# Kernel optimization log

Hardware: AMD Instinct MI355X
Metric: run time of the kernel (lower is better)

## Reference

```python
import jax, jax.numpy as jnp
import numpy as np

D_MODEL = 1024
NUM_HEADS = 16
B, S = 2, 2048


def setup_inputs() -> dict:
    key = jax.random.key(0)
    ks = jax.random.split(key, 11)
    scale = 1.0 / np.sqrt(D_MODEL)
    inp = {
        'q': jax.random.normal(ks[0], (B, S, D_MODEL), jnp.float32),
        'k': jax.random.normal(ks[1], (B, S, D_MODEL), jnp.float32),
        'v': jax.random.normal(ks[2], (B, S, D_MODEL), jnp.float32),
        'w_q': jax.random.normal(ks[3], (D_MODEL, D_MODEL), jnp.float32) * scale,
        'b_q': jax.random.normal(ks[4], (D_MODEL,), jnp.float32) * 0.01,
        'w_k': jax.random.normal(ks[5], (D_MODEL, D_MODEL), jnp.float32) * scale,
        'b_k': jax.random.normal(ks[6], (D_MODEL,), jnp.float32) * 0.01,
        'w_v': jax.random.normal(ks[7], (D_MODEL, D_MODEL), jnp.float32) * scale,
        'b_v': jax.random.normal(ks[8], (D_MODEL,), jnp.float32) * 0.01,
        'w_o': jax.random.normal(ks[9], (D_MODEL, D_MODEL), jnp.float32) * scale,
        'b_o': jax.random.normal(ks[10], (D_MODEL,), jnp.float32) * 0.01,
    }
    return inp


def reference(q, k, v, w_q, b_q, w_k, b_k, w_v, b_v, w_o, b_o):
    Bq, Sq, D = q.shape
    H = NUM_HEADS
    dh = D // H
    # projections (weights stored as [in, out])
    query = q @ w_q + b_q
    key = k @ w_k + b_k
    value = v @ w_v + b_v
    # [B, S, D] -> [B, H, S, dh]
    query = query.reshape(Bq, Sq, H, dh).transpose(0, 2, 1, 3)
    key = key.reshape(Bq, -1, H, dh).transpose(0, 2, 1, 3)
    value = value.reshape(Bq, -1, H, dh).transpose(0, 2, 1, 3)
    # NOTE: original module does NOT scale by 1/sqrt(dh)
    scores = jnp.einsum('bhqd,bhkd->bhqk', query, key)  # [B,H,S,S]
    causal_mask = jnp.triu(jnp.ones((Sq, Sq), dtype=bool), k=1)  # True above diag
    scores = jnp.where(causal_mask[None, None], -jnp.inf, scores)
    attn = jax.nn.softmax(scores, axis=-1)
    data = jnp.einsum('bhqk,bhkd->bhqd', attn, value)  # [B,H,S,dh]
    # FAITHFUL to original bug: transpose(0,1) then view(B, S, -1)
    data = data.transpose(1, 0, 2, 3).reshape(Bq, Sq, -1)  # [H,B,S,dh] -> [B,S,D]
    return data @ w_o + b_o
```

## Files before the change

kernel.cpp:

```cpp
#include <hip/hip_runtime.h>

typedef __fp16 f16;
typedef __fp16 f16x8 __attribute__((ext_vector_type(8)));
typedef __fp16 f16x4 __attribute__((ext_vector_type(4)));
typedef __fp16 f16x2 __attribute__((ext_vector_type(2)));
typedef float f32x4 __attribute__((ext_vector_type(4)));
typedef float f32x16 __attribute__((ext_vector_type(16)));

#define D_MODEL 1024
#define SEQ 2048
#define NH 16
#define MTOT 4096

typedef const __attribute__((address_space(1))) unsigned int* gp1_t;
typedef __attribute__((address_space(3))) unsigned int* lp3_t;

__device__ __forceinline__ void gload_lds16(const void* g, void* l) {
  __builtin_amdgcn_global_load_lds((gp1_t)g, (lp3_t)l, 16, 0, 0);
}

__device__ __forceinline__ int permrow(int r) {
  int bp = r >> 11, u = (r >> 7) & 15, t = r & 127;
  int g16 = (bp << 4) | u;
  return ((((g16 & 1) << 4) | (g16 >> 1)) << 7) + t;
}

__device__ __forceinline__ unsigned int pkrtz(float a, float b) {
  union { f16x2 h; unsigned int u; } z;
  z.h = __builtin_amdgcn_cvt_pkrtz(a, b);
  return z.u;
}

__global__ __launch_bounds__(256) void cvt_all(const float* __restrict__ q,
                                               const float* __restrict__ k,
                                               const float* __restrict__ v,
                                               const float* __restrict__ wq,
                                               const float* __restrict__ wk,
                                               const float* __restrict__ wv,
                                               const float* __restrict__ wo,
                                               f16* __restrict__ qkv16,
                                               f16* __restrict__ wT) {
  __shared__ float tl[64][65];
  int bid = blockIdx.x, tid = threadIdx.x;
  if (bid < 6144) {
    int i = bid * 256 + tid;
    const int NT = (MTOT * D_MODEL) / 8;
    const float* src;
    int t;
    if (i < NT) { src = q; t = i; }
    else if (i < 2 * NT) { src = k; t = i - NT; }
    else { src = v; t = i - 2 * NT; }
    const float4* s4 = (const float4*)src;
    float4 a = s4[2 * t], b = s4[2 * t + 1];
    f16x8 h;
    h[0] = (f16)a.x; h[1] = (f16)a.y; h[2] = (f16)a.z; h[3] = (f16)a.w;
    h[4] = (f16)b.x; h[5] = (f16)b.y; h[6] = (f16)b.z; h[7] = (f16)b.w;
    *(f16x8*)(qkv16 + (size_t)i * 8) = h;
  } else {
    int bb = bid - 6144;
    int mat = bb >> 8, tile = bb & 255;
    int tk = (tile >> 4) << 6, tn = (tile & 15) << 6;
    const float* W = mat == 0 ? wq : mat == 1 ? wk : mat == 2 ? wv : wo;
    int rr = tid >> 4, c4 = (tid & 15) << 2;
#pragma unroll
    for (int it = 0; it < 4; ++it) {
      const float* p = W + (size_t)(tk + it * 16 + rr) * D_MODEL + tn + c4;
      float4 val = *(const float4*)p;
      tl[it * 16 + rr][c4 + 0] = val.x;
      tl[it * 16 + rr][c4 + 1] = val.y;
      tl[it * 16 + rr][c4 + 2] = val.z;
      tl[it * 16 + rr][c4 + 3] = val.w;
    }
    __syncthreads();
    int n = tid & 63, kseg = (tid >> 6) << 4;
    f16x8 lo, hi;
#pragma unroll
    for (int j = 0; j < 8; ++j) lo[j] = (f16)tl[kseg + j][n];
#pragma unroll
    for (int j = 0; j < 8; ++j) hi[j] = (f16)tl[kseg + 8 + j][n];
    f16* d = wT + (size_t)mat * (D_MODEL * D_MODEL) + (size_t)(tn + n) * D_MODEL + tk + kseg;
    *(f16x8*)d = lo;
    *(f16x8*)(d + 8) = hi;
  }
}

__global__ __launch_bounds__(256, 2) void gemm_qkv(const f16* __restrict__ q16,
                                                   const f16* __restrict__ k16,
                                                   const f16* __restrict__ v16,
                                                   const f16* __restrict__ wT,
                                                   const float* __restrict__ bq,
                                                   const float* __restrict__ bk,
                                                   const float* __restrict__ bv,
                                                   f16* __restrict__ Q16,
                                                   f16* __restrict__ K16,
                                                   f16* __restrict__ VT16) {
  const int K = D_MODEL, N = D_MODEL;
  const size_t WEL = (size_t)D_MODEL * D_MODEL;
  int z = blockIdx.z;
  const f16* A = z == 0 ? q16 : z == 1 ? k16 : v16;
  const f16* BT = wT + (size_t)z * WEL;
  const float* bias = z == 0 ? bq : z == 1 ? bk : bv;

  __shared__ f16 As[128 * 64];
  __shared__ f16 Bs[128 * 64];
  int tid = threadIdx.x;
  int w = tid >> 6, lane = tid & 63;
  int g = lane >> 4, c = lane & 15;
  int wr = w >> 1, wc = w & 1;
  int m0 = blockIdx.x * 128, n0 = blockIdx.y * 128;
  f32x4 acc[4][4] = {};

  for (int kt = 0; kt < K; kt += 64) {
#pragma unroll
    for (int i = 0; i < 4; ++i) {
      int seg = w * 4 + i;
      int p = seg * 1024 + lane * 16;
      int row = p >> 7;
      int colb = (p & 127) ^ ((row & 7) << 4);
      int ae = kt + (colb >> 1);
      gload_lds16(A + (size_t)(m0 + row) * K + ae, &As[seg * 512]);
      gload_lds16(BT + (size_t)(n0 + row) * K + ae, &Bs[seg * 512]);
    }
    __syncthreads();
    f16x8 af[4][2], bf[4][2];
#pragma unroll
    for (int m = 0; m < 4; ++m) {
#pragma unroll
      for (int kk = 0; kk < 2; ++kk) {
        int row = wr * 64 + m * 16 + c;
        int tb = (row * 128 + kk * 64 + g * 16) ^ ((row & 7) << 4);
        af[m][kk] = *(const f16x8*)((const char*)As + tb);
      }
    }
#pragma unroll
    for (int n = 0; n < 4; ++n) {
#pragma unroll
      for (int kk = 0; kk < 2; ++kk) {
        int row = wc * 64 + n * 16 + c;
        int tb = (row * 128 + kk * 64 + g * 16) ^ ((row & 7) << 4);
        bf[n][kk] = *(const f16x8*)((const char*)Bs + tb);
      }
    }
    __builtin_amdgcn_s_setprio(1);
#pragma unroll
    for (int m = 0; m < 4; ++m)
#pragma unroll
      for (int n = 0; n < 4; ++n)
#pragma unroll
        for (int kk = 0; kk < 2; ++kk)
          acc[m][n] = __builtin_amdgcn_mfma_f32_16x16x32_f16(af[m][kk], bf[n][kk], acc[m][n], 0, 0, 0);
    __builtin_amdgcn_s_setprio(0);
    __syncthreads();
  }

  int rb = m0 + wr * 64;
  int cb = n0 + wc * 64;
  if (z < 2) {
    f16* O = z == 0 ? Q16 : K16;
#pragma unroll
    for (int m = 0; m < 4; ++m) {
      int row0 = rb + m * 16 + 4 * g;
#pragma unroll
      for (int n = 0; n < 4; ++n) {
        int col = cb + n * 16 + c;
        float bv2 = bias[col];
#pragma unroll
        for (int r = 0; r < 4; ++r) O[(size_t)(row0 + r) * N + col] = (f16)(acc[m][n][r] + bv2);
      }
    }
  } else {
    f16* O = VT16;
#pragma unroll
    for (int m = 0; m < 4; ++m) {
      int s0f = rb + m * 16 + 4 * g;
      int bb = s0f >> 11, s = s0f & (SEQ - 1);
#pragma unroll
      for (int n = 0; n < 4; ++n) {
        int col = cb + n * 16 + c;
        float bv2 = bias[col];
        f16x4 hv;
#pragma unroll
        for (int r = 0; r < 4; ++r) hv[r] = (f16)(acc[m][n][r] + bv2);
        *(f16x4*)(O + ((size_t)(bb * NH + (col >> 6)) * 64 + (col & 63)) * SEQ + s) = hv;
      }
    }
  }
}

__global__ __launch_bounds__(256, 2) void gemm_out(const f16* __restrict__ A,
                                                   const f16* __restrict__ BT,
                                                   const float* __restrict__ bias,
                                                   float* __restrict__ O) {
  const int K = D_MODEL, N = D_MODEL;
  __shared__ f16 As[64 * 64];
  __shared__ f16 Bs[128 * 64];
  int tid = threadIdx.x;
  int w = tid >> 6, lane = tid & 63;
  int g = lane >> 4, c = lane & 15;
  int wr = w >> 1, wc = w & 1;
  int m0 = blockIdx.x * 64, n0 = blockIdx.y * 128;
  f32x4 acc[2][4] = {};

  for (int kt = 0; kt < K; kt += 64) {
#pragma unroll
    for (int i = 0; i < 2; ++i) {
      int seg = w * 2 + i;
      int p = seg * 1024 + lane * 16;
      int row = p >> 7;
      int colb = (p & 127) ^ ((row & 7) << 4);
      int ae = kt + (colb >> 1);
      gload_lds16(A + (size_t)permrow(m0 + row) * K + ae, &As[seg * 512]);
    }
#pragma unroll
    for (int i = 0; i < 4; ++i) {
      int seg = w * 4 + i;
      int p = seg * 1024 + lane * 16;
      int row = p >> 7;
      int colb = (p & 127) ^ ((row & 7) << 4);
      int ae = kt + (colb >> 1);
      gload_lds16(BT + (size_t)(n0 + row) * K + ae, &Bs[seg * 512]);
    }
    __syncthreads();
    f16x8 af[2][2], bf[4][2];
#pragma unroll
    for (int m = 0; m < 2; ++m) {
#pragma unroll
      for (int kk = 0; kk < 2; ++kk) {
        int row = wr * 32 + m * 16 + c;
        int tb = (row * 128 + kk * 64 + g * 16) ^ ((row & 7) << 4);
        af[m][kk] = *(const f16x8*)((const char*)As + tb);
      }
    }
#pragma unroll
    for (int n = 0; n < 4; ++n) {
#pragma unroll
      for (int kk = 0; kk < 2; ++kk) {
        int row = wc * 64 + n * 16 + c;
        int tb = (row * 128 + kk * 64 + g * 16) ^ ((row & 7) << 4);
        bf[n][kk] = *(const f16x8*)((const char*)Bs + tb);
      }
    }
    __builtin_amdgcn_s_setprio(1);
#pragma unroll
    for (int m = 0; m < 2; ++m)
#pragma unroll
      for (int n = 0; n < 4; ++n)
#pragma unroll
        for (int kk = 0; kk < 2; ++kk)
          acc[m][n] = __builtin_amdgcn_mfma_f32_16x16x32_f16(af[m][kk], bf[n][kk], acc[m][n], 0, 0, 0);
    __builtin_amdgcn_s_setprio(0);
    __syncthreads();
  }

  int rb = m0 + wr * 32;
  int cb = n0 + wc * 64;
#pragma unroll
  for (int m = 0; m < 2; ++m) {
    int row0 = rb + m * 16 + 4 * g;
#pragma unroll
    for (int n = 0; n < 4; ++n) {
      int col = cb + n * 16 + c;
      float bv = bias[col];
#pragma unroll
      for (int r = 0; r < 4; ++r) O[(size_t)(row0 + r) * N + col] = acc[m][n][r] + bv;
    }
  }
}

#define THR2 11.5f
__global__ __launch_bounds__(128, 2) void attn_kernel(const f16* __restrict__ Q,
                                                      const f16* __restrict__ K,
                                                      const f16* __restrict__ VT,
                                                      f16* __restrict__ AO) {
  __shared__ __attribute__((aligned(16))) f16 Ksh[2][64 * 64];
  __shared__ __attribute__((aligned(16))) f16 Vsh[2][64 * 64];
  int tid = threadIdx.x;
  int w = tid >> 6, lane = tid & 63;
  int c = lane & 31, hi = lane >> 5;
  int blk = blockIdx.x;
  int bh = blk & 31;
  int uu = blk >> 5;
  int grp = uu & 7, pos = uu >> 3;
  int cb = pos == 0 ? grp : pos == 1 ? 15 - grp : pos == 2 ? 16 + grp : 31 - grp;
  int b = bh >> 4, h = bh & 15;
  int q0 = cb * 64 + w * 32;
  const int NT = cb + 1;
  const size_t brow = (size_t)b * SEQ;
  const int hcol = h * 64;

  int sr = lane >> 3;
  int seo = ((lane & 7) ^ sr) << 3;
  const f16* Kgb = K + (size_t)(brow + w * 32 + sr) * D_MODEL + hcol + seo;
  const f16* Vgb = VT + ((size_t)bh * 64 + w * 32 + sr) * SEQ + seo;

  const f16 LOG2E = (f16)1.44269504f;
  f16x8 qf[4];
  const f16* Qp = Q + (size_t)(brow + q0 + c) * D_MODEL + hcol + 8 * hi;
#pragma unroll
  for (int kk = 0; kk < 4; ++kk) {
    qf[kk] = *(const f16x8*)(Qp + 16 * kk);
#pragma unroll
    for (int j = 0; j < 8; ++j) qf[kk][j] = (f16)(qf[kk][j] * LOG2E);
  }

  float m_st = -1e30f, l_st = 0.f;
  f32x16 o0 = {}, o1 = {};

#pragma unroll
  for (int j = 0; j < 4; ++j) {
    gload_lds16(Kgb + (size_t)(j * 8) * D_MODEL, &Ksh[0][(w * 32 + j * 8) * 64]);
    gload_lds16(Vgb + (size_t)(j * 8) * SEQ, &Vsh[0][(w * 32 + j * 8) * 64]);
  }
  __syncthreads();

  int rsw = (c & 7) << 4;
  int cur = 0;
  for (int t = 0; t < NT; ++t) {
    if (t + 1 < NT) {
      int kv1 = (t + 1) * 64;
      int nx = cur ^ 1;
#pragma unroll
      for (int j = 0; j < 4; ++j) {
        gload_lds16(Kgb + (size_t)(kv1 + j * 8) * D_MODEL, &Ksh[nx][(w * 32 + j * 8) * 64]);
        gload_lds16(Vgb + (size_t)(j * 8) * SEQ + kv1, &Vsh[nx][(w * 32 + j * 8) * 64]);
      }
    }
    const char* Kb = (const char*)&Ksh[cur][0];
    const char* Vb = (const char*)&Vsh[cur][0];
    f16x8 kf[2][4];
#pragma unroll
    for (int ks = 0; ks < 2; ++ks)
#pragma unroll
      for (int kk = 0; kk < 4; ++kk)
        kf[ks][kk] = *(const f16x8*)(Kb + (((ks * 32 + c) * 128 + 32 * kk + 16 * hi) ^ rsw));
    f32x16 s0 = {}, s1 = {};
    __builtin_amdgcn_s_setprio(1);
#pragma unroll
    for (int kk = 0; kk < 4; ++kk) {
      s0 = __builtin_amdgcn_mfma_f32_32x32x16_f16(kf[0][kk], qf[kk], s0, 0, 0, 0);
      s1 = __builtin_amdgcn_mfma_f32_32x32x16_f16(kf[1][kk], qf[kk], s1, 0, 0, 0);
    }
    __builtin_amdgcn_s_setprio(0);
    if (t == NT - 1) {
      int q = q0 + c;
      int kvb = t * 64 + 4 * hi;
#pragma unroll
      for (int r = 0; r < 16; ++r) {
        int kv = kvb + (r & 3) + 8 * (r >> 2);
        if (kv > q) s0[r] = -1e30f;
        if (kv + 32 > q) s1[r] = -1e30f;
      }
    }
    float t8[8];
#pragma unroll
    for (int r = 0; r < 8; ++r)
      t8[r] = fmaxf(fmaxf(s0[r], s0[r + 8]), fmaxf(s1[r], s1[r + 8]));
    float pm = fmaxf(fmaxf(fmaxf(t8[0], t8[1]), fmaxf(t8[2], t8[3])),
                     fmaxf(fmaxf(t8[4], t8[5]), fmaxf(t8[6], t8[7])));
    float mx = fmaxf(pm, __shfl_xor(pm, 32));
    if (__any(mx > m_st + THR2)) {
      float mnew = fmaxf(m_st, mx);
      float corr = __builtin_amdgcn_exp2f(m_st - mnew);
      l_st *= corr;
#pragma unroll
      for (int r = 0; r < 16; ++r) { o0[r] *= corr; o1[r] *= corr; }
      m_st = mnew;
    }
    float lacc = 0.f;
#pragma unroll
    for (int r = 0; r < 16; ++r) {
      float p0 = __builtin_amdgcn_exp2f(s0[r] - m_st);
      float p1 = __builtin_amdgcn_exp2f(s1[r] - m_st);
      s0[r] = p0; s1[r] = p1;
      lacc += p0 + p1;
    }
    l_st += lacc;
    union PU { unsigned int u[4]; f16x8 v; };
    PU pu[4];
#pragma unroll
    for (int kk = 0; kk < 4; ++kk) {
      int rb = 8 * (kk & 1);
      unsigned int la0, la1, lb0, lb1;
      if (kk < 2) {
        la0 = pkrtz(s0[rb + 0], s0[rb + 1]);
        la1 = pkrtz(s0[rb + 2], s0[rb + 3]);
        lb0 = pkrtz(s0[rb + 4], s0[rb + 5]);
        lb1 = pkrtz(s0[rb + 6], s0[rb + 7]);
      } else {
        la0 = pkrtz(s1[rb + 0], s1[rb + 1]);
        la1 = pkrtz(s1[rb + 2], s1[rb + 3]);
        lb0 = pkrtz(s1[rb + 4], s1[rb + 5]);
        lb1 = pkrtz(s1[rb + 6], s1[rb + 7]);
      }
      asm("v_permlane32_swap_b32 %0, %1" : "+v"(la0), "+v"(lb0));
      asm("v_permlane32_swap_b32 %0, %1" : "+v"(la1), "+v"(lb1));
      pu[kk].u[0] = la0; pu[kk].u[1] = la1; pu[kk].u[2] = lb0; pu[kk].u[3] = lb1;
    }
    f16x8 vf[2][4];
#pragma unroll
    for (int dt = 0; dt < 2; ++dt)
#pragma unroll
      for (int kk = 0; kk < 4; ++kk)
        vf[dt][kk] = *(const f16x8*)(Vb + (((dt * 32 + c) * 128 + 32 * kk + 16 * hi) ^ rsw));
    __builtin_amdgcn_s_setprio(1);
#pragma unroll
    for (int kk = 0; kk < 4; ++kk) {
      o0 = __builtin_amdgcn_mfma_f32_32x32x16_f16(vf[0][kk], pu[kk].v, o0, 0, 0, 0);
      o1 = __builtin_amdgcn_mfma_f32_32x32x16_f16(vf[1][kk], pu[kk].v, o1, 0, 0, 0);
    }
    __builtin_amdgcn_s_setprio(0);
    __syncthreads();
    cur ^= 1;
  }

  float lt = l_st + __shfl_xor(l_st, 32);
  float linv = 1.0f / lt;
  f16* aoq = AO + ((size_t)bh * SEQ + q0 + c) * 64 + 4 * hi;
#pragma unroll
  for (int rq = 0; rq < 4; ++rq) {
    f16x4 h0, h1;
#pragma unroll
    for (int r = 0; r < 4; ++r) {
      h0[r] = (f16)(o0[4 * rq + r] * linv);
      h1[r] = (f16)(o1[4 * rq + r] * linv);
    }
    *(f16x4*)(aoq + 8 * rq) = h0;
    *(f16x4*)(aoq + 32 + 8 * rq) = h1;
  }
}

extern "C" void kernel_launch(void* const* d_in, const int* in_sizes, int n_in,
                              void* d_out, int out_size, void* d_ws, size_t ws_size,
                              hipStream_t stream) {
  const float* q  = (const float*)d_in[0];
  const float* k  = (const float*)d_in[1];
  const float* v  = (const float*)d_in[2];
  const float* wq = (const float*)d_in[3];
  const float* bq = (const float*)d_in[4];
  const float* wk = (const float*)d_in[5];
  const float* bk = (const float*)d_in[6];
  const float* wv = (const float*)d_in[7];
  const float* bv = (const float*)d_in[8];
  const float* wo = (const float*)d_in[9];
  const float* bo = (const float*)d_in[10];

  const size_t TEN = (size_t)MTOT * D_MODEL;
  const size_t WEL = (size_t)D_MODEL * D_MODEL;
  f16* ws  = (f16*)d_ws;
  f16* q16 = ws;
  f16* k16 = q16 + TEN;
  f16* v16 = k16 + TEN;
  f16* wT  = v16 + TEN;
  f16* Q16 = wT + 4 * WEL;
  f16* K16 = Q16 + TEN;
  f16* VT16 = K16 + TEN;
  f16* AO  = q16;

  cvt_all<<<7168, 256, 0, stream>>>(q, k, v, wq, wk, wv, wo, q16, wT);
  gemm_qkv<<<dim3(32, 8, 3), 256, 0, stream>>>(q16, k16, v16, wT, bq, bk, bv, Q16, K16, VT16);
  attn_kernel<<<1024, 128, 0, stream>>>(Q16, K16, VT16, AO);
  gemm_out<<<dim3(64, 8), 256, 0, stream>>>(AO, wT + 3 * WEL, bo, (float*)d_out);
}
```

Baseline: 122.6 us.

## Split attention KV loop across two wave pairs with LDS merge of partial softmax

Each attention block now runs four waves: two query halves times two KV parities, so even and odd KV tiles are processed concurrently by separate waves and combined at the end through an LDS merge of running max, sum and output. Block scheduling drops the interleaved causal-block ordering in favour of longest-first (cb = 31 - uu), the row-sum reduction becomes a tree, and V fragment loads move before the softmax. This is meant to shorten the serial KV chain per block and raise the number of waves per CU. In exchange it doubles LDS per block, adds a final sync and merge step, and leaves idle waves when the tile count is odd.

```diff
diff --git a/kernel.cpp b/kernel.cpp
--- a/kernel.cpp
+++ b/kernel.cpp
@@ -268,30 +268,35 @@
 }
 
 #define THR2 11.5f
-__global__ __launch_bounds__(128, 2) void attn_kernel(const f16* __restrict__ Q,
+__global__ __launch_bounds__(256, 2) void attn_kernel(const f16* __restrict__ Q,
                                                       const f16* __restrict__ K,
                                                       const f16* __restrict__ VT,
                                                       f16* __restrict__ AO) {
-  __shared__ __attribute__((aligned(16))) f16 Ksh[2][64 * 64];
-  __shared__ __attribute__((aligned(16))) f16 Vsh[2][64 * 64];
+  __shared__ __attribute__((aligned(16))) f16 Ksh[2][2][64 * 64];
+  __shared__ __attribute__((aligned(16))) f16 Vsh[2][2][64 * 64];
+  const int BUFO = 2 * 64 * 64;
   int tid = threadIdx.x;
   int w = tid >> 6, lane = tid & 63;
   int c = lane & 31, hi = lane >> 5;
+  int qh = w & 1, par = w >> 1;
   int blk = blockIdx.x;
   int bh = blk & 31;
   int uu = blk >> 5;
-  int grp = uu & 7, pos = uu >> 3;
-  int cb = pos == 0 ? grp : pos == 1 ? 15 - grp : pos == 2 ? 16 + grp : 31 - grp;
+  int cb = 31 - uu;
   int b = bh >> 4, h = bh & 15;
-  int q0 = cb * 64 + w * 32;
+  int q0 = cb * 64 + qh * 32;
   const int NT = cb + 1;
   const size_t brow = (size_t)b * SEQ;
   const int hcol = h * 64;
 
   int sr = lane >> 3;
   int seo = ((lane & 7) ^ sr) << 3;
-  const f16* Kgb = K + (size_t)(brow + w * 32 + sr) * D_MODEL + hcol + seo;
-  const f16* Vgb = VT + ((size_t)bh * 64 + w * 32 + sr) * SEQ + seo;
+  const f16* Kgb = K + (size_t)(brow + qh * 32 + sr) * D_MODEL + hcol + seo;
+  const f16* Vgb = VT + ((size_t)bh * 64 + qh * 32 + sr) * SEQ + seo;
+  f16* Kshf = &Ksh[0][0][0];
+  f16* Vshf = &Vsh[0][0][0];
+  f16* KshW = Kshf + par * 4096 + qh * 32 * 64;
+  f16* VshW = Vshf + par * 4096 + qh * 32 * 64;
 
   const f16 LOG2E = (f16)1.44269504f;
   f16x8 qf[4];
@@ -306,126 +311,160 @@
   float m_st = -1e30f, l_st = 0.f;
   f32x16 o0 = {}, o1 = {};
 
-#pragma unroll
-  for (int j = 0; j < 4; ++j) {
-    gload_lds16(Kgb + (size_t)(j * 8) * D_MODEL, &Ksh[0][(w * 32 + j * 8) * 64]);
-    gload_lds16(Vgb + (size_t)(j * 8) * SEQ, &Vsh[0][(w * 32 + j * 8) * 64]);
+  if (par < NT) {
+    int kv = par * 64;
+#pragma unroll
+    for (int j = 0; j < 4; ++j) {
+      gload_lds16(Kgb + (size_t)(kv + j * 8) * D_MODEL, KshW + (j * 8) * 64);
+      gload_lds16(Vgb + (size_t)(j * 8) * SEQ + kv, VshW + (j * 8) * 64);
+    }
   }
   __syncthreads();
 
   int rsw = (c & 7) << 4;
   int cur = 0;
-  for (int t = 0; t < NT; ++t) {
-    if (t + 1 < NT) {
-      int kv1 = (t + 1) * 64;
-      int nx = cur ^ 1;
+  const int U = (NT + 1) >> 1;
+  for (int u = 0; u < U; ++u) {
+    int tpre = 2 * u + 2 + par;
+    if (tpre < NT) {
+      int kv = tpre * 64;
+      f16* kd = KshW + (cur ^ 1) * BUFO;
+      f16* vd = VshW + (cur ^ 1) * BUFO;
 #pragma unroll
       for (int j = 0; j < 4; ++j) {
-        gload_lds16(Kgb + (size_t)(kv1 + j * 8) * D_MODEL, &Ksh[nx][(w * 32 + j * 8) * 64]);
-        gload_lds16(Vgb + (size_t)(j * 8) * SEQ + kv1, &Vsh[nx][(w * 32 + j * 8) * 64]);
-      }
-    }
-    const char* Kb = (const char*)&Ksh[cur][0];
-    const char* Vb = (const char*)&Vsh[cur][0];
-    f16x8 kf[2][4];
-#pragma unroll
-    for (int ks = 0; ks < 2; ++ks)
-#pragma unroll
-      for (int kk = 0; kk < 4; ++kk)
-        kf[ks][kk] = *(const f16x8*)(Kb + (((ks * 32 + c) * 128 + 32 * kk + 16 * hi) ^ rsw));
-    f32x16 s0 = {}, s1 = {};
-    __builtin_amdgcn_s_setprio(1);
-#pragma unroll
-    for (int kk = 0; kk < 4; ++kk) {
-      s0 = __builtin_amdgcn_mfma_f32_32x32x16_f16(kf[0][kk], qf[kk], s0, 0, 0, 0);
-      s1 = __builtin_amdgcn_mfma_f32_32x32x16_f16(kf[1][kk], qf[kk], s1, 0, 0, 0);
-    }
-    __builtin_amdgcn_s_setprio(0);
-    if (t == NT - 1) {
-      int q = q0 + c;
-      int kvb = t * 64 + 4 * hi;
+        gload_lds16(Kgb + (size_t)(kv + j * 8) * D_MODEL, kd + (j * 8) * 64);
+        gload_lds16(Vgb + (size_t)(j * 8) * SEQ + kv, vd + (j * 8) * 64);
+      }
+    }
+    int t = 2 * u + par;
+    if (t < NT) {
+      const char* Kb = (const char*)(Kshf + cur * BUFO + par * 4096);
+      const char* Vb = (const char*)(Vshf + cur * BUFO + par * 4096);
+      f16x8 kf[2][4];
+#pragma unroll
+      for (int ks = 0; ks < 2; ++ks)
+#pragma unroll
+        for (int kk = 0; kk < 4; ++kk)
+          kf[ks][kk] = *(const f16x8*)(Kb + (((ks * 32 + c) * 128 + 32 * kk + 16 * hi) ^ rsw));
+      f32x16 s0 = {}, s1 = {};
+      __builtin_amdgcn_s_setprio(1);
+#pragma unroll
+      for (int kk = 0; kk < 4; ++kk) {
+        s0 = __builtin_amdgcn_mfma_f32_32x32x16_f16(kf[0][kk], qf[kk], s0, 0, 0, 0);
+        s1 = __builtin_amdgcn_mfma_f32_32x32x16_f16(kf[1][kk], qf[kk], s1, 0, 0, 0);
+      }
+      __builtin_amdgcn_s_setprio(0);
+      f16x8 vf[2][4];
+#pragma unroll
+      for (int dt = 0; dt < 2; ++dt)
+#pragma unroll
+        for (int kk = 0; kk < 4; ++kk)
+          vf[dt][kk] = *(const f16x8*)(Vb + (((dt * 32 + c) * 128 + 32 * kk + 16 * hi) ^ rsw));
+      if (t == NT - 1) {
+        int q = q0 + c;
+        int kvb = t * 64 + 4 * hi;
+#pragma unroll
+        for (int r = 0; r < 16; ++r) {
+          int kv = kvb + (r & 3) + 8 * (r >> 2);
+          if (kv > q) s0[r] = -1e30f;
+          if (kv + 32 > q) s1[r] = -1e30f;
+        }
+      }
+      float t8[8];
+#pragma unroll
+      for (int r = 0; r < 8; ++r)
+        t8[r] = fmaxf(fmaxf(s0[r], s0[r + 8]), fmaxf(s1[r], s1[r + 8]));
+      float pm = fmaxf(fmaxf(fmaxf(t8[0], t8[1]), fmaxf(t8[2], t8[3])),
+                       fmaxf(fmaxf(t8[4], t8[5]), fmaxf(t8[6], t8[7])));
+      float mx = fmaxf(pm, __shfl_xor(pm, 32));
+      if (__any(mx > m_st + THR2)) {
+        float mnew = fmaxf(m_st, mx);
+        float corr = __builtin_amdgcn_exp2f(m_st - mnew);
+        l_st *= corr;
+#pragma unroll
+        for (int r = 0; r < 16; ++r) { o0[r] *= corr; o1[r] *= corr; }
+        m_st = mnew;
+      }
+      float ts[16];
 #pragma unroll
       for (int r = 0; r < 16; ++r) {
-        int kv = kvb + (r & 3) + 8 * (r >> 2);
-        if (kv > q) s0[r] = -1e30f;
-        if (kv + 32 > q) s1[r] = -1e30f;
-      }
-    }
-    float t8[8];
-#pragma unroll
-    for (int r = 0; r < 8; ++r)
-      t8[r] = fmaxf(fmaxf(s0[r], s0[r + 8]), fmaxf(s1[r], s1[r + 8]));
-    float pm = fmaxf(fmaxf(fmaxf(t8[0], t8[1]), fmaxf(t8[2], t8[3])),
-                     fmaxf(fmaxf(t8[4], t8[5]), fmaxf(t8[6], t8[7])));
-    float mx = fmaxf(pm, __shfl_xor(pm, 32));
-    if (__any(mx > m_st + THR2)) {
-      float mnew = fmaxf(m_st, mx);
-      float corr = __builtin_amdgcn_exp2f(m_st - mnew);
-      l_st *= corr;
-#pragma unroll
-      for (int r = 0; r < 16; ++r) { o0[r] *= corr; o1[r] *= corr; }
-      m_st = mnew;
-    }
-    float lacc = 0.f;
-#pragma unroll
-    for (int r = 0; r < 16; ++r) {
-      float p0 = __builtin_amdgcn_exp2f(s0[r] - m_st);
-      float p1 = __builtin_amdgcn_exp2f(s1[r] - m_st);
-      s0[r] = p0; s1[r] = p1;
-      lacc += p0 + p1;
-    }
-    l_st += lacc;
-    union PU { unsigned int u[4]; f16x8 v; };
-    PU pu[4];
-#pragma unroll
-    for (int kk = 0; kk < 4; ++kk) {
-      int rb = 8 * (kk & 1);
-      unsigned int la0, la1, lb0, lb1;
-      if (kk < 2) {
-        la0 = pkrtz(s0[rb + 0], s0[rb + 1]);
-        la1 = pkrtz(s0[rb + 2], s0[rb + 3]);
-        lb0 = pkrtz(s0[rb + 4], s0[rb + 5]);
-        lb1 = pkrtz(s0[rb + 6], s0[rb + 7]);
-      } else {
-        la0 = pkrtz(s1[rb + 0], s1[rb + 1]);
-        la1 = pkrtz(s1[rb + 2], s1[rb + 3]);
-        lb0 = pkrtz(s1[rb + 4], s1[rb + 5]);
-        lb1 = pkrtz(s1[rb + 6], s1[rb + 7]);
-      }
-      asm("v_permlane32_swap_b32 %0, %1" : "+v"(la0), "+v"(lb0));
-      asm("v_permlane32_swap_b32 %0, %1" : "+v"(la1), "+v"(lb1));
-      pu[kk].u[0] = la0; pu[kk].u[1] = la1; pu[kk].u[2] = lb0; pu[kk].u[3] = lb1;
-    }
-    f16x8 vf[2][4];
-#pragma unroll
-    for (int dt = 0; dt < 2; ++dt)
-#pragma unroll
-      for (int kk = 0; kk < 4; ++kk)
-        vf[dt][kk] = *(const f16x8*)(Vb + (((dt * 32 + c) * 128 + 32 * kk + 16 * hi) ^ rsw));
-    __builtin_amdgcn_s_setprio(1);
-#pragma unroll
-    for (int kk = 0; kk < 4; ++kk) {
-      o0 = __builtin_amdgcn_mfma_f32_32x32x16_f16(vf[0][kk], pu[kk].v, o0, 0, 0, 0);
-      o1 = __builtin_amdgcn_mfma_f32_32x32x16_f16(vf[1][kk], pu[kk].v, o1, 0, 0, 0);
-    }
-    __builtin_amdgcn_s_setprio(0);
+        float p0 = __builtin_amdgcn_exp2f(s0[r] - m_st);
+        float p1 = __builtin_amdgcn_exp2f(s1[r] - m_st);
+        s0[r] = p0; s1[r] = p1;
+        ts[r] = p0 + p1;
+      }
+#pragma unroll
+      for (int st = 8; st > 0; st >>= 1)
+#pragma unroll
+        for (int r = 0; r < st; ++r) ts[r] += ts[r + st];
+      l_st += ts[0];
+      union PU { unsigned int u[4]; f16x8 v; };
+      PU pu[4];
+#pragma unroll
+      for (int kk = 0; kk < 4; ++kk) {
+        int rb = 8 * (kk & 1);
+        unsigned int la0, la1, lb0, lb1;
+        if (kk < 2) {
+          la0 = pkrtz(s0[rb + 0], s0[rb + 1]);
+          la1 = pkrtz(s0[rb + 2], s0[rb + 3]);
+          lb0 = pkrtz(s0[rb + 4], s0[rb + 5]);
+          lb1 = pkrtz(s0[rb + 6], s0[rb + 7]);
+        } else {
+          la0 = pkrtz(s1[rb + 0], s1[rb + 1]);
+          la1 = pkrtz(s1[rb + 2], s1[rb + 3]);
+          lb0 = pkrtz(s1[rb + 4], s1[rb + 5]);
+          lb1 = pkrtz(s1[rb + 6], s1[rb + 7]);
+        }
+        asm("v_permlane32_swap_b32 %0, %1" : "+v"(la0), "+v"(lb0));
+        asm("v_permlane32_swap_b32 %0, %1" : "+v"(la1), "+v"(lb1));
+        pu[kk].u[0] = la0; pu[kk].u[1] = la1; pu[kk].u[2] = lb0; pu[kk].u[3] = lb1;
+      }
+      __builtin_amdgcn_s_setprio(1);
+#pragma unroll
+      for (int kk = 0; kk < 4; ++kk) {
+        o0 = __builtin_amdgcn_mfma_f32_32x32x16_f16(vf[0][kk], pu[kk].v, o0, 0, 0, 0);
+        o1 = __builtin_amdgcn_mfma_f32_32x32x16_f16(vf[1][kk], pu[kk].v, o1, 0, 0, 0);
+      }
+      __builtin_amdgcn_s_setprio(0);
+    }
     __syncthreads();
     cur ^= 1;
   }
 
-  float lt = l_st + __shfl_xor(l_st, 32);
-  float linv = 1.0f / lt;
-  f16* aoq = AO + ((size_t)bh * SEQ + q0 + c) * 64 + 4 * hi;
-#pragma unroll
-  for (int rq = 0; rq < 4; ++rq) {
-    f16x4 h0, h1;
-#pragma unroll
-    for (int r = 0; r < 4; ++r) {
-      h0[r] = (f16)(o0[4 * rq + r] * linv);
-      h1[r] = (f16)(o1[4 * rq + r] * linv);
-    }
-    *(f16x4*)(aoq + 8 * rq) = h0;
-    *(f16x4*)(aoq + 32 + 8 * rq) = h1;
+  float* sc = (float*)Kshf;
+  int mb = (qh * 64 + lane) * 34;
+  if (par == 1) {
+    sc[mb] = m_st;
+    sc[mb + 1] = l_st;
+#pragma unroll
+    for (int r = 0; r < 16; ++r) { sc[mb + 2 + r] = o0[r]; sc[mb + 18 + r] = o1[r]; }
+  }
+  __syncthreads();
+  if (par == 0) {
+    float m1 = sc[mb], l1 = sc[mb + 1];
+    float mm = fmaxf(m_st, m1);
+    float c0 = __builtin_amdgcn_exp2f(m_st - mm);
+    float c1 = __builtin_amdgcn_exp2f(m1 - mm);
+    float l = l_st * c0 + l1 * c1;
+#pragma unroll
+    for (int r = 0; r < 16; ++r) {
+      o0[r] = o0[r] * c0 + sc[mb + 2 + r] * c1;
+      o1[r] = o1[r] * c0 + sc[mb + 18 + r] * c1;
+    }
+    float lt = l + __shfl_xor(l, 32);
+    float linv = 1.0f / lt;
+    f16* aoq = AO + ((size_t)bh * SEQ + q0 + c) * 64 + 4 * hi;
+#pragma unroll
+    for (int rq = 0; rq < 4; ++rq) {
+      f16x4 h0, h1;
+#pragma unroll
+      for (int r = 0; r < 4; ++r) {
+        h0[r] = (f16)(o0[4 * rq + r] * linv);
+        h1[r] = (f16)(o1[4 * rq + r] * linv);
+      }
+      *(f16x4*)(aoq + 8 * rq) = h0;
+      *(f16x4*)(aoq + 32 + 8 * rq) = h1;
+    }
   }
 }
 
@@ -458,6 +497,6 @@
 
   cvt_all<<<7168, 256, 0, stream>>>(q, k, v, wq, wk, wv, wo, q16, wT);
   gemm_qkv<<<dim3(32, 8, 3), 256, 0, stream>>>(q16, k16, v16, wT, bq, bk, bv, Q16, K16, VT16);
-  attn_kernel<<<1024, 128, 0, stream>>>(Q16, K16, VT16, AO);
+  attn_kernel<<<1024, 256, 0, stream>>>(Q16, K16, VT16, AO);
   gemm_out<<<dim3(64, 8), 256, 0, stream>>>(AO, wT + 3 * WEL, bo, (float*)d_out);
 }
```

Result: faster. 110.8 us (-9.7%).
